# Performance work log

Measured on AMD Instinct MI355X. Metric: run time of the kernel, lower is better.

## Reference

```python
import jax, jax.numpy as jnp
import numpy as np

N_HEADS = 16
N_KV_HEADS = 4
HEAD_DIM = 128  # d_model // n_heads = 2048 // 16
ROPE_THETA = 10000.0


def _rope_cos_sin(T, D, dtype):
    inv_freq = 1.0 / (ROPE_THETA ** (jnp.arange(0, D, 2, dtype=jnp.float32) / D))
    t = jnp.arange(T, dtype=jnp.float32)
    freqs = jnp.outer(t, inv_freq)               # [T, D/2]
    emb = jnp.concatenate([freqs, freqs], axis=-1)  # [T, D]
    return jnp.cos(emb).astype(dtype), jnp.sin(emb).astype(dtype)


def _rotate_half(x):
    x1, x2 = jnp.split(x, 2, axis=-1)
    return jnp.concatenate([-x2, x1], axis=-1)


def setup_inputs() -> dict:
    key = jax.random.key(0)
    k1, k2, k3, k4, k5 = jax.random.split(key, 5)
    B, T, C = 2, 2048, 2048
    H, KV, D = N_HEADS, N_KV_HEADS, HEAD_DIM
    s = 0.02
    return {
        "x": jax.random.normal(k1, (B, T, C), dtype=jnp.float32),
        "Wq": jax.random.normal(k2, (C, H * D), dtype=jnp.float32) * s,
        "Wk": jax.random.normal(k3, (C, KV * D), dtype=jnp.float32) * s,
        "Wv": jax.random.normal(k4, (C, KV * D), dtype=jnp.float32) * s,
        "Wo": jax.random.normal(k5, (H * D, C), dtype=jnp.float32) * s,
    }


def reference(x, Wq, Wk, Wv, Wo):
    B, T, C = x.shape
    H, KV, D = N_HEADS, N_KV_HEADS, HEAD_DIM
    G = H // KV
    scale = D ** -0.5

    q = (x @ Wq).reshape(B, T, H, D).transpose(0, 2, 1, 3)    # [B,H,T,D]
    k = (x @ Wk).reshape(B, T, KV, D).transpose(0, 2, 1, 3)   # [B,KV,T,D]
    v = (x @ Wv).reshape(B, T, KV, D).transpose(0, 2, 1, 3)   # [B,KV,T,D]

    cos, sin = _rope_cos_sin(T, D, x.dtype)  # [T,D] each, broadcasts over B,H
    q = q * cos + _rotate_half(q) * sin
    k = k * cos + _rotate_half(k) * sin

    # repeat_interleave kv heads to match query heads
    k = jnp.repeat(k, G, axis=1)  # [B,H,T,D]
    v = jnp.repeat(v, G, axis=1)  # [B,H,T,D]

    scores = jnp.einsum('bhqd,bhkd->bhqk', q, k) * scale  # [B,H,T,T]
    causal = jnp.tril(jnp.ones((T, T), dtype=bool))
    scores = jnp.where(causal, scores, jnp.finfo(scores.dtype).min)
    attn = jax.nn.softmax(scores, axis=-1)

    out = jnp.einsum('bhqk,bhkd->bhqd', attn, v)           # [B,H,T,D]
    out = out.transpose(0, 2, 1, 3).reshape(B, T, H * D)    # [B,T,C]
    return out @ Wo
```

## Files before the change

### kernel.cpp

```cpp
#include <hip/hip_runtime.h>
#include <cstdint>
#include <cstddef>

typedef __attribute__((ext_vector_type(4))) float f32x4;
typedef __attribute__((ext_vector_type(8))) short s16x8;
typedef __attribute__((ext_vector_type(4))) short s16x4;

#define B_  2
#define T_  2048
#define C_  2048
#define H_  16
#define KV_ 4
#define D_  128
#define M_  4096

static __device__ __forceinline__ float bf2f(ushort u){
  union { float f; uint32_t u; } x; x.u = ((uint32_t)u) << 16; return x.f;
}
static __device__ __forceinline__ ushort f2bf(float f){
  union { float f; uint32_t u; } x; x.f = f;
  uint32_t r = x.u + 0x7FFF + ((x.u >> 16) & 1);
  return (ushort)(r >> 16);
}

static __device__ __forceinline__ void gl_lds16(const ushort* g, ushort* s){
  __builtin_amdgcn_global_load_lds((const __attribute__((address_space(1))) void*)g,
                                   (__attribute__((address_space(3))) void*)s, 16, 0, 0);
}

__global__ void cvt_f32_bf16(const float* __restrict__ in, ushort* __restrict__ out, int n4){
  int idx = blockIdx.x * blockDim.x + threadIdx.x;
  int stride = gridDim.x * blockDim.x;
  for (int i = idx; i < n4; i += stride){
    float4 v = ((const float4*)in)[i];
    s16x4 o;
    o[0] = (short)f2bf(v.x); o[1] = (short)f2bf(v.y);
    o[2] = (short)f2bf(v.z); o[3] = (short)f2bf(v.w);
    ((s16x4*)out)[i] = o;
  }
}

__global__ void transpose_cvt(const float* __restrict__ W, ushort* __restrict__ Wt, int K, int N){
  __shared__ float tile[32][33];
  int n0 = blockIdx.x * 32, k0 = blockIdx.y * 32;
  int tx = threadIdx.x, ty = threadIdx.y;
  #pragma unroll
  for (int r = 0; r < 4; r++)
    tile[ty + 8*r][tx] = W[(size_t)(k0 + ty + 8*r) * N + n0 + tx];
  __syncthreads();
  #pragma unroll
  for (int r = 0; r < 4; r++)
    Wt[(size_t)(n0 + ty + 8*r) * K + k0 + tx] = f2bf(tile[tx][ty + 8*r]);
}

template<int MODE, int BN>
__global__ __launch_bounds__(512)
void gemm_v2(const ushort* __restrict__ A, const ushort* __restrict__ Bt,
             void* __restrict__ C0, void* __restrict__ C1, void* __restrict__ C2,
             int N, int Kd){
  constexpr int NF = BN / 32;
  constexpr int BV = BN / 64;
  __shared__ __align__(16) ushort Abuf[2][16384];
  __shared__ __align__(16) ushort Bbuf[2][BN * 64];
  int tid = threadIdx.x, w = tid >> 6, l = tid & 63;
  int l15 = l & 15, l4 = l >> 4;

  int x = blockIdx.x & 7, i = blockIdx.x >> 3;
  int by = (x & 3) * 4 + (i & 3);
  int bx = (x >> 2) * 8 + (i >> 2);
  int rblk = by * 256, cblk = bx * BN;
  int wm = w >> 1, wn = w & 1;

  int sr = tid >> 3;
  int sc = ((tid & 7) * 8) ^ ((sr & 7) << 3);
  const ushort* gA = A  + (size_t)(rblk + sr) * Kd + sc;
  const ushort* gB = Bt + (size_t)(cblk + sr) * Kd + sc;
  int wb = w * 512;

  auto stage = [&](int t){
    int cur = t & 1; int koff = t * 64;
    #pragma unroll
    for (int v = 0; v < 4; v++)
      gl_lds16(gA + (size_t)v * 64 * Kd + koff, &Abuf[cur][v * 4096 + wb]);
    #pragma unroll
    for (int v = 0; v < BV; v++)
      gl_lds16(gB + (size_t)v * 64 * Kd + koff, &Bbuf[cur][v * 4096 + wb]);
  };

  int arow = wm * 64 + l15;
  int brow = wn * (BN / 2) + l15;
  int sw = (l15 & 7) << 3;
  int kx0 = (l4 * 8) ^ sw;
  int kx1 = (32 + l4 * 8) ^ sw;

  f32x4 acc[4][NF] = {};

  stage(0);
  asm volatile("s_waitcnt vmcnt(0)" ::: "memory");
  __builtin_amdgcn_s_barrier();

  int nt = Kd >> 6;
  for (int t = 0; t < nt; ++t){
    if (t + 1 < nt) stage(t + 1);
    const ushort* Ab = Abuf[t & 1];
    const ushort* Bb = Bbuf[t & 1];
    s16x8 a[4][2], b[NF][2];
    #pragma unroll
    for (int m = 0; m < 4; m++){
      a[m][0] = *(const s16x8*)(Ab + (arow + m*16) * 64 + kx0);
      a[m][1] = *(const s16x8*)(Ab + (arow + m*16) * 64 + kx1);
    }
    #pragma unroll
    for (int n = 0; n < NF; n++){
      b[n][0] = *(const s16x8*)(Bb + (brow + n*16) * 64 + kx0);
      b[n][1] = *(const s16x8*)(Bb + (brow + n*16) * 64 + kx1);
    }
    asm volatile("s_waitcnt lgkmcnt(0)" ::: "memory");
    __builtin_amdgcn_sched_barrier(0);
    __builtin_amdgcn_s_setprio(1);
    #pragma unroll
    for (int m = 0; m < 4; m++)
      #pragma unroll
      for (int n = 0; n < NF; n++){
        acc[m][n] = __builtin_amdgcn_mfma_f32_16x16x32_bf16(a[m][0], b[n][0], acc[m][n], 0, 0, 0);
        acc[m][n] = __builtin_amdgcn_mfma_f32_16x16x32_bf16(a[m][1], b[n][1], acc[m][n], 0, 0, 0);
      }
    __builtin_amdgcn_s_setprio(0);
    if (t + 1 < nt){
      asm volatile("s_waitcnt vmcnt(0)" ::: "memory");
      __builtin_amdgcn_sched_barrier(0);
      __builtin_amdgcn_s_barrier();
    }
  }

  #pragma unroll
  for (int m = 0; m < 4; m++){
    #pragma unroll
    for (int n = 0; n < NF; n++){
      #pragma unroll
      for (int j = 0; j < 4; j++){
        int row = rblk + wm*64 + m*16 + l4*4 + j;
        int col = cblk + wn*(BN/2) + n*16 + l15;
        float v = acc[m][n][j];
        if (MODE == 0){
          ((float*)C0)[(size_t)row * N + col] = v;
        } else {
          int t = row & (T_ - 1), bb = row >> 11;
          ushort bv = f2bf(v);
          if (col < 2048){
            int hh = col >> 7, d = col & 127;
            ((ushort*)C0)[(((size_t)(bb * H_ + hh)) * T_ + t) * D_ + d] = bv;
          } else if (col < 2560){
            int c2 = col - 2048;
            int hh = c2 >> 7, d = c2 & 127;
            ((ushort*)C1)[(((size_t)(bb * KV_ + hh)) * T_ + t) * D_ + d] = bv;
          } else {
            int c2 = col - 2560;
            int hh = c2 >> 7, d = c2 & 127;
            ((ushort*)C2)[(((size_t)(bb * KV_ + hh)) * D_ + d) * T_ + t] = bv;
          }
        }
      }
    }
  }
}

__global__ __launch_bounds__(256)
void rope_inplace2(ushort* __restrict__ X, float scale){
  int tr = threadIdx.x >> 4;
  int j  = threadIdx.x & 15;
  int t  = blockIdx.x * 16 + tr;
  int bh = blockIdx.y;
  ushort* row = X + ((size_t)bh * T_ + t) * D_;
  s16x4 lo = *(const s16x4*)(row + j*4);
  s16x4 hi = *(const s16x4*)(row + 64 + j*4);
  s16x4 olo, ohi;
  #pragma unroll
  for (int i = 0; i < 4; i++){
    int d = j*4 + i;
    float invf = exp2f(-(float)d * 0.2076205059304602f);
    float s, c;
    __sincosf((float)t * invf, &s, &c);
    float q1 = bf2f((ushort)lo[i]);
    float q2 = bf2f((ushort)hi[i]);
    olo[i] = (short)f2bf((q1 * c - q2 * s) * scale);
    ohi[i] = (short)f2bf((q2 * c + q1 * s) * scale);
  }
  *(s16x4*)(row + j*4) = olo;
  *(s16x4*)(row + 64 + j*4) = ohi;
}

__global__ __launch_bounds__(512, 4)
void attn_kernel4(const ushort* __restrict__ Q, const ushort* __restrict__ Kc,
                  const ushort* __restrict__ Vt, ushort* __restrict__ O){
  __shared__ __align__(16) ushort Ks[64 * 128];
  __shared__ __align__(16) ushort Vs[128 * 64];
  __shared__ __align__(16) ushort Ps[8 * 16 * 64];
  int bid = blockIdx.x;
  int i  = bid >> 3;
  int qt = (i < 32) ? (63 - i) : (i - 32);
  int sub = bid & 7;
  int b = sub >> 2, kvh = sub & 3;
  int tid = threadIdx.x, w = tid >> 6, l = tid & 63;
  int l15 = l & 15, l4 = l >> 4;
  int sw3 = (l15 & 7) << 3;
  int q0 = qt * 32;
  int hq = kvh * 4 + (w >> 1);
  int qrow0 = q0 + (w & 1) * 16;
  int qrow = qrow0 + l15;

  s16x8 qf[4];
  const ushort* qbase = Q + (((size_t)(b * H_ + hq)) * T_ + qrow) * D_;
  #pragma unroll
  for (int kk = 0; kk < 4; kk++)
    qf[kk] = *(const s16x8*)(qbase + kk * 32 + l4 * 8);

  f32x4 oacc[8] = {};
  float mrun = -1e30f;
  float rsum = 0.f;
  const float THR = 11.5415603f;
  ushort* Pw = Ps + w * (16 * 64) + l15 * 64;

  const ushort* kbase = Kc + ((size_t)(b * KV_ + kvh)) * T_ * D_;
  const ushort* vbase = Vt + ((size_t)(b * KV_ + kvh)) * D_ * T_;
  int jmax = (q0 + 31) >> 6;

  int kr0 = tid >> 4, kcb = tid & 15;
  int vd0 = tid >> 3, vtb = tid & 7;
  int ksoff = kr0 * 128 + ((kcb * 8) ^ ((kr0 & 7) << 3));
  int vsoff = vd0 * 64  + ((vtb * 8) ^ ((vd0 & 7) << 3));
  const ushort* kg = kbase + (size_t)kr0 * D_ + kcb * 8;
  const ushort* vg = vbase + (size_t)vd0 * T_ + vtb * 8;

  s16x8 kreg0, kreg1, vreg0, vreg1;
  kreg0 = *(const s16x8*)(kg);
  kreg1 = *(const s16x8*)(kg + (size_t)32 * D_);
  vreg0 = *(const s16x8*)(vg);
  vreg1 = *(const s16x8*)(vg + (size_t)64 * T_);

  for (int jt = 0; jt <= jmax; jt++){
    __syncthreads();
    *(s16x8*)(Ks + ksoff)            = kreg0;
    *(s16x8*)(Ks + ksoff + 32 * 128) = kreg1;
    *(s16x8*)(Vs + vsoff)            = vreg0;
    *(s16x8*)(Vs + vsoff + 64 * 64)  = vreg1;
    __syncthreads();
    if (jt < jmax){
      int k1 = (jt + 1) * 64;
      kreg0 = *(const s16x8*)(kg + (size_t)k1 * D_);
      kreg1 = *(const s16x8*)(kg + (size_t)(k1 + 32) * D_);
      vreg0 = *(const s16x8*)(vg + k1);
      vreg1 = *(const s16x8*)(vg + (size_t)64 * T_ + k1);
    }
    int k0 = jt * 64;

    f32x4 sacc[4] = {};
    __builtin_amdgcn_s_setprio(1);
    #pragma unroll
    for (int kk = 0; kk < 4; kk++){
      #pragma unroll
      for (int n = 0; n < 4; n++){
        s16x8 kf = *(const s16x8*)(Ks + (16*n + l15) * 128 + ((kk*32 + l4*8) ^ sw3));
        sacc[n] = __builtin_amdgcn_mfma_f32_16x16x32_bf16(kf, qf[kk], sacc[n], 0, 0, 0);
      }
    }
    __builtin_amdgcn_s_setprio(0);
    if (jt == jmax){
      #pragma unroll
      for (int n = 0; n < 4; n++)
        #pragma unroll
        for (int j = 0; j < 4; j++){
          int kcol = k0 + 16*n + 4*l4 + j;
          if (kcol > qrow) sacc[n][j] = -1e30f;
        }
    }
    float mloc = -1e30f;
    #pragma unroll
    for (int n = 0; n < 4; n++)
      #pragma unroll
      for (int j = 0; j < 4; j++)
        mloc = fmaxf(mloc, sacc[n][j]);
    if (__any((int)(mloc > mrun + THR))){
      float m2 = fmaxf(mloc, __shfl_xor(mloc, 16));
      m2 = fmaxf(m2, __shfl_xor(m2, 32));
      float mnew = fmaxf(mrun, m2);
      float alpha = exp2f(mrun - mnew);
      mrun = mnew;
      rsum *= alpha;
      #pragma unroll
      for (int n8 = 0; n8 < 8; n8++)
        #pragma unroll
        for (int j = 0; j < 4; j++)
          oacc[n8][j] *= alpha;
    }
    #pragma unroll
    for (int n = 0; n < 4; n++){
      s16x4 pk;
      #pragma unroll
      for (int j = 0; j < 4; j++){
        float p = exp2f(sacc[n][j] - mrun);
        rsum += p;
        pk[j] = (short)f2bf(p);
      }
      *(s16x4*)(Pw + ((16*n + 4*l4) ^ sw3)) = pk;
    }
    __builtin_amdgcn_s_setprio(1);
    #pragma unroll
    for (int kk = 0; kk < 2; kk++){
      s16x8 pf = *(const s16x8*)(Pw + ((kk*32 + l4*8) ^ sw3));
      #pragma unroll
      for (int n8 = 0; n8 < 8; n8++){
        s16x8 vf = *(const s16x8*)(Vs + (16*n8 + l15) * 64 + ((kk*32 + l4*8) ^ sw3));
        oacc[n8] = __builtin_amdgcn_mfma_f32_16x16x32_bf16(vf, pf, oacc[n8], 0, 0, 0);
      }
    }
    __builtin_amdgcn_s_setprio(0);
  }

  rsum += __shfl_xor(rsum, 16);
  rsum += __shfl_xor(rsum, 32);
  float inv = 1.f / rsum;
  ushort* obase = O + ((size_t)(b * T_ + qrow)) * C_ + hq * D_ + 4*l4;
  #pragma unroll
  for (int n8 = 0; n8 < 8; n8++){
    s16x4 ov;
    #pragma unroll
    for (int j = 0; j < 4; j++)
      ov[j] = (short)f2bf(oacc[n8][j] * inv);
    *(s16x4*)(obase + 16*n8) = ov;
  }
}

extern "C" void kernel_launch(void* const* d_in, const int* in_sizes, int n_in,
                              void* d_out, int out_size, void* d_ws, size_t ws_size,
                              hipStream_t stream){
  const float* x  = (const float*)d_in[0];
  const float* Wq = (const float*)d_in[1];
  const float* Wk = (const float*)d_in[2];
  const float* Wv = (const float*)d_in[3];
  const float* Wo = (const float*)d_in[4];
  float* out = (float*)d_out;

  char* ws = (char*)d_ws;
  size_t off = 0;
  auto alloc = [&](size_t bytes)->void*{
    void* p = ws + off; off += (bytes + 255) & ~(size_t)255; return p;
  };
  ushort* xb   = (ushort*)alloc((size_t)M_ * C_ * 2);
  ushort* Wcat = (ushort*)alloc((size_t)3072 * 2048 * 2);
  ushort* Wot  = (ushort*)alloc((size_t)2048 * 2048 * 2);
  ushort* Qb   = (ushort*)alloc((size_t)B_ * H_ * T_ * D_ * 2);
  ushort* Kb   = (ushort*)alloc((size_t)B_ * KV_ * T_ * D_ * 2);
  ushort* Vtb  = (ushort*)alloc((size_t)B_ * KV_ * T_ * D_ * 2);
  ushort* Ob   = (ushort*)alloc((size_t)M_ * C_ * 2);

  cvt_f32_bf16<<<2048, 256, 0, stream>>>(x, xb, M_ * C_ / 4);
  transpose_cvt<<<dim3(64, 64), dim3(32, 8), 0, stream>>>(Wq, Wcat, 2048, 2048);
  transpose_cvt<<<dim3(16, 64), dim3(32, 8), 0, stream>>>(Wk, Wcat + (size_t)2048*2048, 2048, 512);
  transpose_cvt<<<dim3(16, 64), dim3(32, 8), 0, stream>>>(Wv, Wcat + (size_t)2560*2048, 2048, 512);
  transpose_cvt<<<dim3(64, 64), dim3(32, 8), 0, stream>>>(Wo, Wot, 2048, 2048);

  gemm_v2<1, 192><<<256, 512, 0, stream>>>(xb, Wcat, Qb, Kb, Vtb, 3072, 2048);

  rope_inplace2<<<dim3(T_/16, B_ * H_),  256, 0, stream>>>(Qb, 0.08838834764831845f * 1.4426950408889634f);
  rope_inplace2<<<dim3(T_/16, B_ * KV_), 256, 0, stream>>>(Kb, 1.0f);

  attn_kernel4<<<512, 512, 0, stream>>>(Qb, Kb, Vtb, Ob);

  gemm_v2<0, 128><<<256, 512, 0, stream>>>(Ob, Wot, out, nullptr, nullptr, 2048, 2048);
}
```

Baseline: 223.3 us.

## Rework projection GEMMs with triple-buffered LDS pipeline and new tile shapes

Replaces the double-buffered GEMM with a three-stage LDS ring that prefetches two K-tiles ahead and waits with partial vmcnt counts, so a load stays in flight across the barrier. Block tiles change to 128 rows, with the QKV GEMM using 512 blocks of 128x192 and the output GEMM using 128x256. Warps are laid out 2x4 instead of 4x2, and a linear XCD-aware block remapping replaces the previous swizzle. This trades more LDS per block and smaller M tiles, which lowers per-block reuse, for deeper latency hiding and more blocks on the QKV projection.

```diff
diff --git a/kernel.cpp b/kernel.cpp
--- a/kernel.cpp
+++ b/kernel.cpp
@@ -26,6 +26,13 @@
 static __device__ __forceinline__ void gl_lds16(const ushort* g, ushort* s){
   __builtin_amdgcn_global_load_lds((const __attribute__((address_space(1))) void*)g,
                                    (__attribute__((address_space(3))) void*)s, 16, 0, 0);
+}
+
+template<int N> __device__ __forceinline__ void vmw(){
+  if constexpr (N == 0)      asm volatile("s_waitcnt vmcnt(0)" ::: "memory");
+  else if constexpr (N == 5) asm volatile("s_waitcnt vmcnt(5)" ::: "memory");
+  else if constexpr (N == 6) asm volatile("s_waitcnt vmcnt(6)" ::: "memory");
+  __builtin_amdgcn_sched_barrier(0);
 }
 
 __global__ void cvt_f32_bf16(const float* __restrict__ in, ushort* __restrict__ out, int n4){
@@ -55,21 +62,22 @@
 
 template<int MODE, int BN>
 __global__ __launch_bounds__(512)
-void gemm_v2(const ushort* __restrict__ A, const ushort* __restrict__ Bt,
+void gemm_d2(const ushort* __restrict__ A, const ushort* __restrict__ Bt,
              void* __restrict__ C0, void* __restrict__ C1, void* __restrict__ C2,
              int N, int Kd){
-  constexpr int NF = BN / 32;
-  constexpr int BV = BN / 64;
-  __shared__ __align__(16) ushort Abuf[2][16384];
-  __shared__ __align__(16) ushort Bbuf[2][BN * 64];
+  constexpr int NF  = BN / 64;
+  constexpr int BV  = BN / 64;
+  constexpr int LPT = 2 + BV;
+  __shared__ __align__(16) ushort Ab[3][8192];
+  __shared__ __align__(16) ushort Bb[3][BN * 64];
   int tid = threadIdx.x, w = tid >> 6, l = tid & 63;
   int l15 = l & 15, l4 = l >> 4;
 
-  int x = blockIdx.x & 7, i = blockIdx.x >> 3;
-  int by = (x & 3) * 4 + (i & 3);
-  int bx = (x >> 2) * 8 + (i >> 2);
-  int rblk = by * 256, cblk = bx * BN;
-  int wm = w >> 1, wn = w & 1;
+  int cpx = gridDim.x >> 3;
+  int logical = (blockIdx.x & 7) * cpx + (blockIdx.x >> 3);
+  int by = logical & 31, bx = logical >> 5;
+  int rblk = by * 128, cblk = bx * BN;
+  int wm = w >> 2, wn = w & 3;
 
   int sr = tid >> 3;
   int sc = ((tid & 7) * 8) ^ ((sr & 7) << 3);
@@ -77,43 +85,44 @@
   const ushort* gB = Bt + (size_t)(cblk + sr) * Kd + sc;
   int wb = w * 512;
 
-  auto stage = [&](int t){
-    int cur = t & 1; int koff = t * 64;
-    #pragma unroll
-    for (int v = 0; v < 4; v++)
-      gl_lds16(gA + (size_t)v * 64 * Kd + koff, &Abuf[cur][v * 4096 + wb]);
+  auto stage = [&](int t, int sb){
+    int koff = t * 64;
+    #pragma unroll
+    for (int v = 0; v < 2; v++)
+      gl_lds16(gA + (size_t)(v * 64) * Kd + koff, &Ab[sb][v * 4096 + wb]);
     #pragma unroll
     for (int v = 0; v < BV; v++)
-      gl_lds16(gB + (size_t)v * 64 * Kd + koff, &Bbuf[cur][v * 4096 + wb]);
+      gl_lds16(gB + (size_t)(v * 64) * Kd + koff, &Bb[sb][v * 4096 + wb]);
   };
 
   int arow = wm * 64 + l15;
-  int brow = wn * (BN / 2) + l15;
-  int sw = (l15 & 7) << 3;
-  int kx0 = (l4 * 8) ^ sw;
-  int kx1 = (32 + l4 * 8) ^ sw;
+  int brow = wn * (BN / 4) + l15;
+  int kx0 = (l4 * 8) ^ ((l15 & 7) << 3);
+  int kx1 = (32 + l4 * 8) ^ ((l15 & 7) << 3);
 
   f32x4 acc[4][NF] = {};
 
-  stage(0);
-  asm volatile("s_waitcnt vmcnt(0)" ::: "memory");
+  stage(0, 0); stage(1, 1);
+  vmw<LPT>();
   __builtin_amdgcn_s_barrier();
 
   int nt = Kd >> 6;
+  #pragma unroll 1
   for (int t = 0; t < nt; ++t){
-    if (t + 1 < nt) stage(t + 1);
-    const ushort* Ab = Abuf[t & 1];
-    const ushort* Bb = Bbuf[t & 1];
+    int sb = t % 3;
+    if (t + 2 < nt) stage(t + 2, (t + 2) % 3);
+    const ushort* Abuf = Ab[sb];
+    const ushort* Bbuf = Bb[sb];
     s16x8 a[4][2], b[NF][2];
     #pragma unroll
     for (int m = 0; m < 4; m++){
-      a[m][0] = *(const s16x8*)(Ab + (arow + m*16) * 64 + kx0);
-      a[m][1] = *(const s16x8*)(Ab + (arow + m*16) * 64 + kx1);
+      a[m][0] = *(const s16x8*)(Abuf + (arow + m*16) * 64 + kx0);
+      a[m][1] = *(const s16x8*)(Abuf + (arow + m*16) * 64 + kx1);
     }
     #pragma unroll
     for (int n = 0; n < NF; n++){
-      b[n][0] = *(const s16x8*)(Bb + (brow + n*16) * 64 + kx0);
-      b[n][1] = *(const s16x8*)(Bb + (brow + n*16) * 64 + kx1);
+      b[n][0] = *(const s16x8*)(Bbuf + (brow + n*16) * 64 + kx0);
+      b[n][1] = *(const s16x8*)(Bbuf + (brow + n*16) * 64 + kx1);
     }
     asm volatile("s_waitcnt lgkmcnt(0)" ::: "memory");
     __builtin_amdgcn_sched_barrier(0);
@@ -127,8 +136,7 @@
       }
     __builtin_amdgcn_s_setprio(0);
     if (t + 1 < nt){
-      asm volatile("s_waitcnt vmcnt(0)" ::: "memory");
-      __builtin_amdgcn_sched_barrier(0);
+      if (t + 2 < nt) vmw<LPT>(); else vmw<0>();
       __builtin_amdgcn_s_barrier();
     }
   }
@@ -140,7 +148,7 @@
       #pragma unroll
       for (int j = 0; j < 4; j++){
         int row = rblk + wm*64 + m*16 + l4*4 + j;
-        int col = cblk + wn*(BN/2) + n*16 + l15;
+        int col = cblk + wn*(BN/4) + n*16 + l15;
         float v = acc[m][n][j];
         if (MODE == 0){
           ((float*)C0)[(size_t)row * N + col] = v;
@@ -360,12 +368,12 @@
   transpose_cvt<<<dim3(16, 64), dim3(32, 8), 0, stream>>>(Wv, Wcat + (size_t)2560*2048, 2048, 512);
   transpose_cvt<<<dim3(64, 64), dim3(32, 8), 0, stream>>>(Wo, Wot, 2048, 2048);
 
-  gemm_v2<1, 192><<<256, 512, 0, stream>>>(xb, Wcat, Qb, Kb, Vtb, 3072, 2048);
+  gemm_d2<1, 192><<<512, 512, 0, stream>>>(xb, Wcat, Qb, Kb, Vtb, 3072, 2048);
 
   rope_inplace2<<<dim3(T_/16, B_ * H_),  256, 0, stream>>>(Qb, 0.08838834764831845f * 1.4426950408889634f);
   rope_inplace2<<<dim3(T_/16, B_ * KV_), 256, 0, stream>>>(Kb, 1.0f);
 
   attn_kernel4<<<512, 512, 0, stream>>>(Qb, Kb, Vtb, Ob);
 
-  gemm_v2<0, 128><<<256, 512, 0, stream>>>(Ob, Wot, out, nullptr, nullptr, 2048, 2048);
-}
+  gemm_d2<0, 256><<<256, 512, 0, stream>>>(Ob, Wot, out, nullptr, nullptr, 2048, 2048);
+}
```

Result: slower. 246.6 us (+10.4%).
